# Optimization experiments

Measured on AMD Instinct MI355X. Metric: run time of the kernel, lower is better.

## Reference

```python
import jax, jax.numpy as jnp
import numpy as np

N = 50000
E = 800000
IN_F = 128
HID = 128
OUT_F = 64
MU = 2.0
EPS = 1e-12


def setup_inputs() -> dict:
    key = jax.random.key(0)
    ks = jax.random.split(key, 20)
    d = {}
    d["x"] = jax.random.normal(ks[0], (N, IN_F), dtype=jnp.float32)
    d["edge_src"] = jax.random.randint(ks[1], (E,), 0, N, dtype=jnp.int32)
    d["edge_dst"] = jax.random.randint(ks[2], (E,), 0, N, dtype=jnp.int32)
    d["edge_val"] = jax.random.uniform(ks[3], (E,), dtype=jnp.float32)
    # layer 0: in=128 -> pool=128 -> out=128 (activation=relu)
    s0 = 1.0 / np.sqrt(IN_F)
    d["pool_w0"] = jax.random.uniform(ks[4], (IN_F, IN_F), jnp.float32, -s0, s0)
    d["pool_b0"] = jax.random.uniform(ks[5], (IN_F,), jnp.float32, -s0, s0)
    d["fc1_w0"] = jax.random.uniform(ks[6], (HID, IN_F), jnp.float32, -s0, s0)
    d["fc1_b0"] = jax.random.uniform(ks[7], (HID,), jnp.float32, -s0, s0)
    d["fc2_w0"] = jax.random.uniform(ks[8], (HID, IN_F), jnp.float32, -s0, s0)
    d["fc2_b0"] = jax.random.uniform(ks[9], (HID,), jnp.float32, -s0, s0)
    # layer 1 (final): in=128 -> pool=128 -> out=64 (no activation)
    s1 = 1.0 / np.sqrt(HID)
    d["pool_w1"] = jax.random.uniform(ks[10], (HID, HID), jnp.float32, -s1, s1)
    d["pool_b1"] = jax.random.uniform(ks[11], (HID,), jnp.float32, -s1, s1)
    d["fc1_w1"] = jax.random.uniform(ks[12], (OUT_F, HID), jnp.float32, -s1, s1)
    d["fc1_b1"] = jax.random.uniform(ks[13], (OUT_F,), jnp.float32, -s1, s1)
    d["fc2_w1"] = jax.random.uniform(ks[14], (OUT_F, HID), jnp.float32, -s1, s1)
    d["fc2_b1"] = jax.random.uniform(ks[15], (OUT_F,), jnp.float32, -s1, s1)
    return d


def _sage_conv(x, src, dst, val, pw, pb, w1, b1, w2, b2, act):
    # L2-normalize rows (F.normalize(x, dim=1))
    xn = x / jnp.maximum(jnp.linalg.norm(x, axis=1, keepdims=True), EPS)
    h = jax.nn.relu(xn @ pw.T + pb)               # [N, pool]
    h_mu = h ** MU                                # elementwise pow
    # spmm(adj, h_mu): gather source rows, scale by edge weight, scatter-add to dst rows
    agg = jax.ops.segment_sum(h_mu[src] * val[:, None], dst, num_segments=N)
    agg = agg ** (1.0 / MU)                       # generalized-mean root
    out = (h @ w1.T + b1) + (agg @ w2.T + b2)
    return jax.nn.relu(out) if act else out


def reference(x, edge_src, edge_dst, edge_val,
              pool_w0, pool_b0, fc1_w0, fc1_b0, fc2_w0, fc2_b0,
              pool_w1, pool_b1, fc1_w1, fc1_b1, fc2_w1, fc2_b1):
    h = _sage_conv(x, edge_src, edge_dst, edge_val,
                   pool_w0, pool_b0, fc1_w0, fc1_b0, fc2_w0, fc2_b0, act=True)
    out = _sage_conv(h, edge_src, edge_dst, edge_val,
                     pool_w1, pool_b1, fc1_w1, fc1_b1, fc2_w1, fc2_b1, act=False)
    return out
```

## Files before the change

kernel.cpp:

```cpp
#include <hip/hip_runtime.h>

#define FF 128
#define BCAP 8192
#define CHUNK 4096

typedef __attribute__((ext_vector_type(8))) short short8;
typedef __attribute__((ext_vector_type(4))) float f32x4;

__device__ __forceinline__ unsigned short bf16_rne(float f) {
    unsigned u = __float_as_uint(f);
    u += 0x7fffu + ((u >> 16) & 1u);
    return (unsigned short)(u >> 16);
}
__device__ __forceinline__ float bf16_to_f32(unsigned short h) {
    return __uint_as_float(((unsigned)h) << 16);
}

template<int OUT, int PRE, int ADD, int RELU, int ABF16, int OUTBF16, int OUTSQ>
__global__ __launch_bounds__(256, 2)
void mm_mfma(const void* __restrict__ xin_,
             const unsigned short* __restrict__ Wh, const unsigned short* __restrict__ Wl,
             const float* __restrict__ bias, const float* __restrict__ addsrc,
             void* __restrict__ out_, unsigned short* __restrict__ hsq_out, int N)
{
    constexpr int PITCH = 136;
    __shared__ unsigned short sXh[64 * PITCH];
    __shared__ unsigned short sXl[ABF16 ? 1 : 64 * PITCH];

    const int tid  = threadIdx.x;
    const int tile = blockIdx.x;

    #pragma unroll
    for (int rg = 0; rg < 2; ++rg) {
        const int row = rg * 32 + (tid >> 3);
        const int c0  = (tid & 7) * 16;
        const int n   = tile * 64 + row;
        const int base = row * PITCH + c0;
        if constexpr (ABF16) {
            const unsigned short* xin = (const unsigned short*)xin_;
            short8 a = {0,0,0,0,0,0,0,0}, b = a;
            if (n < N) {
                const short8* p = (const short8*)(xin + (size_t)n * FF + c0);
                a = p[0]; b = p[1];
            }
            *(short8*)&sXh[base]     = a;
            *(short8*)&sXh[base + 8] = b;
        } else {
            const float* xin = (const float*)xin_;
            float v[16];
            if (n < N) {
                const float4* p = (const float4*)(xin + (size_t)n * FF + c0);
                #pragma unroll
                for (int i = 0; i < 4; ++i) {
                    float4 q = p[i];
                    v[4*i] = q.x; v[4*i+1] = q.y; v[4*i+2] = q.z; v[4*i+3] = q.w;
                }
            } else {
                #pragma unroll
                for (int i = 0; i < 16; ++i) v[i] = 0.f;
            }
            if constexpr (PRE == 1) {
                float ss = 0.f;
                #pragma unroll
                for (int i = 0; i < 16; ++i) ss = fmaf(v[i], v[i], ss);
                ss += __shfl_xor(ss, 1);
                ss += __shfl_xor(ss, 2);
                ss += __shfl_xor(ss, 4);
                float scl = 1.0f / fmaxf(sqrtf(ss), 1e-12f);
                #pragma unroll
                for (int i = 0; i < 16; ++i) v[i] *= scl;
            }
            union { unsigned short u[8]; short8 s; } h0, h1, l0, l1;
            #pragma unroll
            for (int i = 0; i < 8; ++i) {
                unsigned short ha = bf16_rne(v[i]);
                unsigned short hb = bf16_rne(v[8 + i]);
                h0.u[i] = ha; h1.u[i] = hb;
                l0.u[i] = bf16_rne(v[i]     - bf16_to_f32(ha));
                l1.u[i] = bf16_rne(v[8 + i] - bf16_to_f32(hb));
            }
            *(short8*)&sXh[base]     = h0.s;
            *(short8*)&sXh[base + 8] = h1.s;
            *(short8*)&sXl[base]     = l0.s;
            *(short8*)&sXl[base + 8] = l1.s;
        }
    }
    __syncthreads();

    const int lane = tid & 63, wave = tid >> 6;
    const int quad = lane >> 4, l16 = lane & 15;
    constexpr int CT = (OUT == 128) ? 2 : 1;

    short8 Bh[CT][4], Bl[CT][4];
    #pragma unroll
    for (int c = 0; c < CT; ++c) {
        const int jt = (OUT == 128) ? (2 * wave + c) : wave;
        #pragma unroll
        for (int t = 0; t < 4; ++t) {
            const size_t o = ((size_t)(jt * 4 + t) * 64 + lane) * 8;
            Bh[c][t] = *(const short8*)&Wh[o];
            Bl[c][t] = *(const short8*)&Wl[o];
        }
    }

    f32x4 acc[4][CT];
    #pragma unroll
    for (int r = 0; r < 4; ++r)
        #pragma unroll
        for (int c = 0; c < CT; ++c) {
            f32x4 z = {0.f, 0.f, 0.f, 0.f};
            acc[r][c] = z;
        }

    #pragma unroll
    for (int t = 0; t < 4; ++t) {
        short8 Ah[4], Al[4];
        #pragma unroll
        for (int r = 0; r < 4; ++r) {
            const int off = (r * 16 + l16) * PITCH + t * 32 + quad * 8;
            Ah[r] = *(const short8*)&sXh[off];
            if constexpr (!ABF16) Al[r] = *(const short8*)&sXl[off];
        }
        #pragma unroll
        for (int c = 0; c < CT; ++c)
            #pragma unroll
            for (int r = 0; r < 4; ++r) {
                acc[r][c] = __builtin_amdgcn_mfma_f32_16x16x32_bf16(Ah[r], Bh[c][t], acc[r][c], 0, 0, 0);
                if constexpr (!ABF16)
                    acc[r][c] = __builtin_amdgcn_mfma_f32_16x16x32_bf16(Al[r], Bh[c][t], acc[r][c], 0, 0, 0);
                acc[r][c] = __builtin_amdgcn_mfma_f32_16x16x32_bf16(Ah[r], Bl[c][t], acc[r][c], 0, 0, 0);
            }
    }

    #pragma unroll
    for (int c = 0; c < CT; ++c) {
        const int jt = (OUT == 128) ? (2 * wave + c) : wave;
        const int j = jt * 16 + l16;
        const float bj = bias[j];
        #pragma unroll
        for (int r = 0; r < 4; ++r) {
            #pragma unroll
            for (int g = 0; g < 4; ++g) {
                const int n = tile * 64 + r * 16 + quad * 4 + g;
                if (n < N) {
                    float val = acc[r][c][g] + bj;
                    if constexpr (ADD) val += addsrc[(size_t)n * OUT + j];
                    if constexpr (RELU) val = fmaxf(val, 0.f);
                    if constexpr (OUTBF16)
                        ((unsigned short*)out_)[(size_t)n * OUT + j] = bf16_rne(val);
                    else
                        ((float*)out_)[(size_t)n * OUT + j] = val;
                    if constexpr (OUTSQ)
                        hsq_out[(size_t)n * OUT + j] = bf16_rne(val * val);
                }
            }
        }
    }
}

template<int OUT, int RELU>
__global__ __launch_bounds__(256, 2)
void mm2_mfma(const unsigned short* __restrict__ hin,
              const unsigned short* __restrict__ aggh,
              const unsigned short* __restrict__ W1h, const unsigned short* __restrict__ W1l,
              const unsigned short* __restrict__ W2h, const unsigned short* __restrict__ W2l,
              const float* __restrict__ b1, const float* __restrict__ b2,
              float* __restrict__ out_, int N)
{
    constexpr int PITCH = 136;
    __shared__ unsigned short sH [64 * PITCH];
    __shared__ unsigned short sAh[64 * PITCH];

    const int tid  = threadIdx.x;
    const int tile = blockIdx.x;

    #pragma unroll
    for (int rg = 0; rg < 2; ++rg) {
        const int row = rg * 32 + (tid >> 3);
        const int c0  = (tid & 7) * 16;
        const int n   = tile * 64 + row;
        const int base = row * PITCH + c0;
        short8 z = {0,0,0,0,0,0,0,0};
        short8 a = z, b = z, c = z, d = z;
        if (n < N) {
            const short8* ph = (const short8*)(hin  + (size_t)n * FF + c0);
            const short8* pa = (const short8*)(aggh + (size_t)n * FF + c0);
            a = ph[0]; b = ph[1];
            c = pa[0]; d = pa[1];
        }
        *(short8*)&sH [base]     = a;
        *(short8*)&sH [base + 8] = b;
        *(short8*)&sAh[base]     = c;
        *(short8*)&sAh[base + 8] = d;
    }
    __syncthreads();

    const int lane = tid & 63, wave = tid >> 6;
    const int quad = lane >> 4, l16 = lane & 15;
    constexpr int CT = (OUT == 128) ? 2 : 1;

    short8 B1hf[CT][4], B1lf[CT][4], B2hf[CT][4], B2lf[CT][4];
    #pragma unroll
    for (int c = 0; c < CT; ++c) {
        const int jt = (OUT == 128) ? (2 * wave + c) : wave;
        #pragma unroll
        for (int t = 0; t < 4; ++t) {
            const size_t o = ((size_t)(jt * 4 + t) * 64 + lane) * 8;
            B1hf[c][t] = *(const short8*)&W1h[o];
            B1lf[c][t] = *(const short8*)&W1l[o];
            B2hf[c][t] = *(const short8*)&W2h[o];
            B2lf[c][t] = *(const short8*)&W2l[o];
        }
    }

    f32x4 acc[4][CT];
    #pragma unroll
    for (int r = 0; r < 4; ++r)
        #pragma unroll
        for (int c = 0; c < CT; ++c) {
            f32x4 z = {0.f, 0.f, 0.f, 0.f};
            acc[r][c] = z;
        }

    #pragma unroll
    for (int t = 0; t < 4; ++t) {
        short8 Hf[4], AH[4];
        #pragma unroll
        for (int r = 0; r < 4; ++r) {
            const int off = (r * 16 + l16) * PITCH + t * 32 + quad * 8;
            Hf[r] = *(const short8*)&sH[off];
            AH[r] = *(const short8*)&sAh[off];
        }
        #pragma unroll
        for (int c = 0; c < CT; ++c)
            #pragma unroll
            for (int r = 0; r < 4; ++r) {
                acc[r][c] = __builtin_amdgcn_mfma_f32_16x16x32_bf16(Hf[r], B1hf[c][t], acc[r][c], 0, 0, 0);
                acc[r][c] = __builtin_amdgcn_mfma_f32_16x16x32_bf16(Hf[r], B1lf[c][t], acc[r][c], 0, 0, 0);
                acc[r][c] = __builtin_amdgcn_mfma_f32_16x16x32_bf16(AH[r], B2hf[c][t], acc[r][c], 0, 0, 0);
                acc[r][c] = __builtin_amdgcn_mfma_f32_16x16x32_bf16(AH[r], B2lf[c][t], acc[r][c], 0, 0, 0);
            }
    }

    #pragma unroll
    for (int c = 0; c < CT; ++c) {
        const int jt = (OUT == 128) ? (2 * wave + c) : wave;
        const int j = jt * 16 + l16;
        const float bj = b1[j] + b2[j];
        #pragma unroll
        for (int r = 0; r < 4; ++r) {
            #pragma unroll
            for (int g = 0; g < 4; ++g) {
                const int n = tile * 64 + r * 16 + quad * 4 + g;
                if (n < N) {
                    float val = acc[r][c][g] + bj;
                    if constexpr (RELU) val = fmaxf(val, 0.f);
                    out_[(size_t)n * OUT + j] = val;
                }
            }
        }
    }
}

struct WPack {
    const float* src[6];
    unsigned short* hi[6];
    unsigned short* lo[6];
    int n[6];
};

__global__ __launch_bounds__(256)
void wprep_kernel(WPack p, int* __restrict__ bucket_cnt)
{
    if (blockIdx.x == 0) bucket_cnt[threadIdx.x] = 0;
    int id = blockIdx.x * 256 + threadIdx.x;
    #pragma unroll
    for (int i = 0; i < 6; ++i) {
        if (id < p.n[i]) {
            float f = p.src[i][id];
            unsigned short h = bf16_rne(f);
            const int j = id >> 7, k = id & 127;
            const int jt = j >> 4, l16 = j & 15;
            const int t = k >> 5, quad = (k >> 3) & 3, j8 = k & 7;
            const size_t o = ((size_t)((jt * 4 + t) * 4 + quad) * 16 + l16) * 8 + j8;
            p.hi[i][o] = h;
            p.lo[i][o] = bf16_rne(f - bf16_to_f32(h));
            return;
        }
        id -= p.n[i];
    }
}

__global__ __launch_bounds__(256)
void partA_kernel(const int* __restrict__ src, const int* __restrict__ dst,
                  const float* __restrict__ val, int* __restrict__ bucket_cnt,
                  int2* __restrict__ ebuf, int E)
{
    __shared__ int cnt[256], sc[256], excl[256], cur[256], gbase[256];
    __shared__ int2 staged[CHUNK];
    const int t = threadIdx.x;
    const int e0 = blockIdx.x * CHUNK;
    const int n  = min(CHUNK, E - e0);

    cnt[t] = 0;
    __syncthreads();
    for (int i = t; i < n; i += 256)
        atomicAdd(&cnt[((unsigned)dst[e0 + i]) >> 8], 1);
    __syncthreads();

    sc[t] = cnt[t];
    __syncthreads();
    #pragma unroll
    for (int off = 1; off < 256; off <<= 1) {
        int v = (t >= off) ? sc[t - off] : 0;
        __syncthreads();
        sc[t] += v;
        __syncthreads();
    }
    excl[t] = sc[t] - cnt[t];
    cur[t]  = excl[t];
    if (cnt[t] > 0) gbase[t] = atomicAdd(&bucket_cnt[t], cnt[t]);
    __syncthreads();

    for (int i = t; i < n; i += 256) {
        int d = dst[e0 + i];
        int s = src[e0 + i];
        float v = val[e0 + i];
        int b = ((unsigned)d) >> 8;
        int slot = atomicAdd(&cur[b], 1);
        staged[slot] = make_int2((s & 0xffff) | (d << 16), __float_as_int(v));
    }
    __syncthreads();

    for (int p = t; p < n; p += 256) {
        int2 ent = staged[p];
        int b = ((unsigned)ent.x) >> 24;
        int gpos = gbase[b] + (p - excl[b]);
        ebuf[(size_t)b * BCAP + gpos] = ent;
    }
}

__global__ __launch_bounds__(256)
void partB_kernel(const int* __restrict__ bucket_cnt, const int2* __restrict__ ebuf,
                  int* __restrict__ offsets, int2* __restrict__ edata,
                  int N, int E, int nbuck)
{
    __shared__ int pre[256], hist[256], sc[256], excl[256], cur[256];
    const int t = threadIdx.x;
    const int b = blockIdx.x;

    pre[t] = (t < nbuck) ? bucket_cnt[t] : 0;
    __syncthreads();
    #pragma unroll
    for (int off = 1; off < 256; off <<= 1) {
        int v = (t >= off) ? pre[t - off] : 0;
        __syncthreads();
        pre[t] += v;
        __syncthreads();
    }
    const int base = (b == 0) ? 0 : pre[b - 1];
    const int cnt  = pre[b] - base;

    hist[t] = 0;
    __syncthreads();
    const int2* ib = ebuf + (size_t)b * BCAP;
    for (int i = t; i < cnt; i += 256)
        atomicAdd(&hist[(((unsigned)ib[i].x) >> 16) & 255], 1);
    __syncthreads();

    sc[t] = hist[t];
    __syncthreads();
    #pragma unroll
    for (int off = 1; off < 256; off <<= 1) {
        int v = (t >= off) ? sc[t - off] : 0;
        __syncthreads();
        sc[t] += v;
        __syncthreads();
    }
    excl[t] = sc[t] - hist[t];
    cur[t]  = excl[t];

    const int node = b * 256 + t;
    if (node <= N) offsets[node] = base + excl[t];
    __syncthreads();

    for (int i = t; i < cnt; i += 256) {
        int2 ent = ib[i];
        int l = (((unsigned)ent.x) >> 16) & 255;
        int pos = base + atomicAdd(&cur[l], 1);
        edata[pos] = make_int2(ent.x & 0xffff, ent.y);
    }
}

__device__ __forceinline__ void fma4(float4& a, float v, uint2 u) {
    a.x = fmaf(v, __uint_as_float(u.x << 16), a.x);
    a.y = fmaf(v, __uint_as_float(u.x & 0xffff0000u), a.y);
    a.z = fmaf(v, __uint_as_float(u.y << 16), a.z);
    a.w = fmaf(v, __uint_as_float(u.y & 0xffff0000u), a.w);
}

__global__ __launch_bounds__(256)
void agg_kernel(const unsigned short* __restrict__ hsq, const int* __restrict__ offsets,
                const int2* __restrict__ edata,
                unsigned short* __restrict__ aggh, int N)
{
    const int w = blockIdx.x * 8 + (threadIdx.x >> 5);
    if (w >= N) return;
    const int l = threadIdx.x & 31;
    const size_t fo = (size_t)(l * 4);
    int e = offsets[w];
    const int end = offsets[w + 1];

    float4 a0 = {0,0,0,0}, a1 = {0,0,0,0}, a2 = {0,0,0,0}, a3 = {0,0,0,0};

    if ((e & 1) && e < end) {
        int2 ed = edata[e];
        uint2 u = *(const uint2*)&hsq[(size_t)ed.x * FF + fo];
        fma4(a0, __int_as_float(ed.y), u);
        ++e;
    }
    for (; e + 3 < end; e += 4) {
        int4 p0 = *(const int4*)&edata[e];
        int4 p1 = *(const int4*)&edata[e + 2];
        uint2 u0 = *(const uint2*)&hsq[(size_t)p0.x * FF + fo];
        uint2 u1 = *(const uint2*)&hsq[(size_t)p0.z * FF + fo];
        uint2 u2 = *(const uint2*)&hsq[(size_t)p1.x * FF + fo];
        uint2 u3 = *(const uint2*)&hsq[(size_t)p1.z * FF + fo];
        fma4(a0, __int_as_float(p0.y), u0);
        fma4(a1, __int_as_float(p0.w), u1);
        fma4(a2, __int_as_float(p1.y), u2);
        fma4(a3, __int_as_float(p1.w), u3);
    }
    if (e + 1 < end) {
        int4 p = *(const int4*)&edata[e];
        uint2 u0 = *(const uint2*)&hsq[(size_t)p.x * FF + fo];
        uint2 u1 = *(const uint2*)&hsq[(size_t)p.z * FF + fo];
        fma4(a0, __int_as_float(p.y), u0);
        fma4(a1, __int_as_float(p.w), u1);
        e += 2;
    }
    if (e < end) {
        int2 ed = edata[e];
        uint2 u = *(const uint2*)&hsq[(size_t)ed.x * FF + fo];
        fma4(a0, __int_as_float(ed.y), u);
    }

    float4 r;
    r.x = sqrtf(a0.x + a1.x + a2.x + a3.x);
    r.y = sqrtf(a0.y + a1.y + a2.y + a3.y);
    r.z = sqrtf(a0.z + a1.z + a2.z + a3.z);
    r.w = sqrtf(a0.w + a1.w + a2.w + a3.w);

    uint2 hv = { (unsigned)bf16_rne(r.x) | ((unsigned)bf16_rne(r.y) << 16),
                 (unsigned)bf16_rne(r.z) | ((unsigned)bf16_rne(r.w) << 16) };
    *(uint2*)&aggh[(size_t)w * FF + fo] = hv;
}

extern "C" void kernel_launch(void* const* d_in, const int* in_sizes, int n_in,
                              void* d_out, int out_size, void* d_ws, size_t ws_size,
                              hipStream_t stream) {
    const float* x    = (const float*)d_in[0];
    const int*   esrc = (const int*)d_in[1];
    const int*   edst = (const int*)d_in[2];
    const float* eval = (const float*)d_in[3];
    const float* pw0  = (const float*)d_in[4];
    const float* pb0  = (const float*)d_in[5];
    const float* f1w0 = (const float*)d_in[6];
    const float* f1b0 = (const float*)d_in[7];
    const float* f2w0 = (const float*)d_in[8];
    const float* f2b0 = (const float*)d_in[9];
    const float* pw1  = (const float*)d_in[10];
    const float* pb1  = (const float*)d_in[11];
    const float* f1w1 = (const float*)d_in[12];
    const float* f1b1 = (const float*)d_in[13];
    const float* f2w1 = (const float*)d_in[14];
    const float* f2b1 = (const float*)d_in[15];
    float* out = (float*)d_out;

    const int N = in_sizes[0] / FF;
    const int E = in_sizes[1];
    const int nbuck = (N + 255) / 256;

    char* ws = (char*)d_ws;
    const size_t rowsz = (size_t)N * FF * sizeof(float);
    const size_t A = 256;
    size_t off = 0;
    unsigned short* h    = (unsigned short*)(ws + off); off += (rowsz / 2 + A - 1) / A * A;
    unsigned short* hsq  = (unsigned short*)(ws + off); off += (rowsz / 2 + A - 1) / A * A;
    unsigned short* aggh = (unsigned short*)(ws + off); off += (rowsz / 2 + A - 1) / A * A;
    float* x1  = (float*)(ws + off); off += rowsz;
    int* offsets = (int*)(ws + off); off += ((size_t)(N + 1) * 4 + A - 1) / A * A;
    int* bucket_cnt = (int*)(ws + off); off += (size_t)256 * 4;
    int2* ebuf  = (int2*)(ws + off); off += (size_t)nbuck * BCAP * 8;
    int2* edata = (int2*)(ws + off); off += (size_t)E * 8;
    const int wsz[6] = {128 * FF, 128 * FF, 128 * FF, 128 * FF, 64 * FF, 64 * FF};
    unsigned short* whi[6];
    unsigned short* wlo[6];
    for (int i = 0; i < 6; ++i) {
        whi[i] = (unsigned short*)(ws + off); off += (size_t)wsz[i] * 2;
        wlo[i] = (unsigned short*)(ws + off); off += (size_t)wsz[i] * 2;
    }

    WPack pack;
    const float* wsrc[6] = {pw0, f1w0, f2w0, pw1, f1w1, f2w1};
    int wtotal = 0;
    for (int i = 0; i < 6; ++i) {
        pack.src[i] = wsrc[i]; pack.hi[i] = whi[i]; pack.lo[i] = wlo[i]; pack.n[i] = wsz[i];
        wtotal += wsz[i];
    }

    const int ntiles     = (N + 63) / 64;
    const int nodeblocks = (N + 7) / 8;
    dim3 B(256);

    wprep_kernel<<<(wtotal + 255) / 256, B, 0, stream>>>(pack, bucket_cnt);

    partA_kernel<<<(E + CHUNK - 1) / CHUNK, B, 0, stream>>>(esrc, edst, eval, bucket_cnt, ebuf, E);
    partB_kernel<<<nbuck, B, 0, stream>>>(bucket_cnt, ebuf, offsets, edata, N, E, nbuck);

    mm_mfma<128, 1, 0, 1, 0, 1, 1><<<ntiles, B, 0, stream>>>(x, whi[0], wlo[0], pb0, nullptr, h, hsq, N);
    agg_kernel<<<nodeblocks, B, 0, stream>>>(hsq, offsets, edata, aggh, N);
    mm2_mfma<128, 1><<<ntiles, B, 0, stream>>>(h, aggh, whi[1], wlo[1], whi[2], wlo[2], f1b0, f2b0, x1, N);

    mm_mfma<128, 1, 0, 1, 0, 1, 1><<<ntiles, B, 0, stream>>>(x1, whi[3], wlo[3], pb1, nullptr, h, hsq, N);
    agg_kernel<<<nodeblocks, B, 0, stream>>>(hsq, offsets, edata, aggh, N);
    mm2_mfma<64, 0><<<ntiles, B, 0, stream>>>(h, aggh, whi[4], wlo[4], whi[5], wlo[5], f1b1, f2b1, out, N);
}
```

Measured before the change: 257.2 us.

## Store layer-1 activations in bf16 and apply row normalization after the matmul

The intermediate layer-0 output x1 is now written as bf16 instead of fp32, halving its write and read traffic. The L2 row normalization moves to the epilogue: per-row inverse norms are kept in shared memory and applied as a scale on the accumulator, so the input is no longer split into hi/lo bf16 parts. This removes one of the three MFMAs per tile step and the low-part shared-memory plane. In exchange the activation input precision drops to single bf16, which adds rounding error.

```diff
diff --git a/kernel.cpp b/kernel.cpp
--- a/kernel.cpp
+++ b/kernel.cpp
@@ -16,16 +16,16 @@
     return __uint_as_float(((unsigned)h) << 16);
 }
 
-template<int OUT, int PRE, int ADD, int RELU, int ABF16, int OUTBF16, int OUTSQ>
+template<int ABF16>
 __global__ __launch_bounds__(256, 2)
-void mm_mfma(const void* __restrict__ xin_,
-             const unsigned short* __restrict__ Wh, const unsigned short* __restrict__ Wl,
-             const float* __restrict__ bias, const float* __restrict__ addsrc,
-             void* __restrict__ out_, unsigned short* __restrict__ hsq_out, int N)
+void pool_mfma(const void* __restrict__ xin_,
+               const unsigned short* __restrict__ Wh, const unsigned short* __restrict__ Wl,
+               const float* __restrict__ bias,
+               unsigned short* __restrict__ hout, unsigned short* __restrict__ hsqout, int N)
 {
     constexpr int PITCH = 136;
-    __shared__ unsigned short sXh[64 * PITCH];
-    __shared__ unsigned short sXl[ABF16 ? 1 : 64 * PITCH];
+    __shared__ unsigned short sX[64 * PITCH];
+    __shared__ float sNorm[64];
 
     const int tid  = threadIdx.x;
     const int tile = blockIdx.x;
@@ -36,15 +36,24 @@
         const int c0  = (tid & 7) * 16;
         const int n   = tile * 64 + row;
         const int base = row * PITCH + c0;
+        float ss = 0.f;
         if constexpr (ABF16) {
             const unsigned short* xin = (const unsigned short*)xin_;
-            short8 a = {0,0,0,0,0,0,0,0}, b = a;
+            union { short8 s; unsigned short u[8]; } a, b;
+            short8 z = {0,0,0,0,0,0,0,0};
+            a.s = z; b.s = z;
             if (n < N) {
                 const short8* p = (const short8*)(xin + (size_t)n * FF + c0);
-                a = p[0]; b = p[1];
-            }
-            *(short8*)&sXh[base]     = a;
-            *(short8*)&sXh[base + 8] = b;
+                a.s = p[0]; b.s = p[1];
+            }
+            #pragma unroll
+            for (int i = 0; i < 8; ++i) {
+                float fa = bf16_to_f32(a.u[i]);
+                float fb = bf16_to_f32(b.u[i]);
+                ss = fmaf(fa, fa, fmaf(fb, fb, ss));
+            }
+            *(short8*)&sX[base]     = a.s;
+            *(short8*)&sX[base + 8] = b.s;
         } else {
             const float* xin = (const float*)xin_;
             float v[16];
@@ -59,42 +68,31 @@
                 #pragma unroll
                 for (int i = 0; i < 16; ++i) v[i] = 0.f;
             }
-            if constexpr (PRE == 1) {
-                float ss = 0.f;
-                #pragma unroll
-                for (int i = 0; i < 16; ++i) ss = fmaf(v[i], v[i], ss);
-                ss += __shfl_xor(ss, 1);
-                ss += __shfl_xor(ss, 2);
-                ss += __shfl_xor(ss, 4);
-                float scl = 1.0f / fmaxf(sqrtf(ss), 1e-12f);
-                #pragma unroll
-                for (int i = 0; i < 16; ++i) v[i] *= scl;
-            }
-            union { unsigned short u[8]; short8 s; } h0, h1, l0, l1;
+            #pragma unroll
+            for (int i = 0; i < 16; ++i) ss = fmaf(v[i], v[i], ss);
+            union { unsigned short u[8]; short8 s; } h0, h1;
             #pragma unroll
             for (int i = 0; i < 8; ++i) {
-                unsigned short ha = bf16_rne(v[i]);
-                unsigned short hb = bf16_rne(v[8 + i]);
-                h0.u[i] = ha; h1.u[i] = hb;
-                l0.u[i] = bf16_rne(v[i]     - bf16_to_f32(ha));
-                l1.u[i] = bf16_rne(v[8 + i] - bf16_to_f32(hb));
-            }
-            *(short8*)&sXh[base]     = h0.s;
-            *(short8*)&sXh[base + 8] = h1.s;
-            *(short8*)&sXl[base]     = l0.s;
-            *(short8*)&sXl[base + 8] = l1.s;
-        }
+                h0.u[i] = bf16_rne(v[i]);
+                h1.u[i] = bf16_rne(v[8 + i]);
+            }
+            *(short8*)&sX[base]     = h0.s;
+            *(short8*)&sX[base + 8] = h1.s;
+        }
+        ss += __shfl_xor(ss, 1);
+        ss += __shfl_xor(ss, 2);
+        ss += __shfl_xor(ss, 4);
+        if ((tid & 7) == 0) sNorm[row] = 1.0f / fmaxf(sqrtf(ss), 1e-12f);
     }
     __syncthreads();
 
     const int lane = tid & 63, wave = tid >> 6;
     const int quad = lane >> 4, l16 = lane & 15;
-    constexpr int CT = (OUT == 128) ? 2 : 1;
-
-    short8 Bh[CT][4], Bl[CT][4];
-    #pragma unroll
-    for (int c = 0; c < CT; ++c) {
-        const int jt = (OUT == 128) ? (2 * wave + c) : wave;
+
+    short8 Bh[2][4], Bl[2][4];
+    #pragma unroll
+    for (int c = 0; c < 2; ++c) {
+        const int jt = 2 * wave + c;
         #pragma unroll
         for (int t = 0; t < 4; ++t) {
             const size_t o = ((size_t)(jt * 4 + t) * 64 + lane) * 8;
@@ -103,69 +101,60 @@
         }
     }
 
-    f32x4 acc[4][CT];
+    f32x4 acc[4][2];
     #pragma unroll
     for (int r = 0; r < 4; ++r)
         #pragma unroll
-        for (int c = 0; c < CT; ++c) {
+        for (int c = 0; c < 2; ++c) {
             f32x4 z = {0.f, 0.f, 0.f, 0.f};
             acc[r][c] = z;
         }
 
     #pragma unroll
     for (int t = 0; t < 4; ++t) {
-        short8 Ah[4], Al[4];
-        #pragma unroll
-        for (int r = 0; r < 4; ++r) {
-            const int off = (r * 16 + l16) * PITCH + t * 32 + quad * 8;
-            Ah[r] = *(const short8*)&sXh[off];
-            if constexpr (!ABF16) Al[r] = *(const short8*)&sXl[off];
-        }
-        #pragma unroll
-        for (int c = 0; c < CT; ++c)
+        short8 Ah[4];
+        #pragma unroll
+        for (int r = 0; r < 4; ++r)
+            Ah[r] = *(const short8*)&sX[(r * 16 + l16) * PITCH + t * 32 + quad * 8];
+        #pragma unroll
+        for (int c = 0; c < 2; ++c)
             #pragma unroll
             for (int r = 0; r < 4; ++r) {
                 acc[r][c] = __builtin_amdgcn_mfma_f32_16x16x32_bf16(Ah[r], Bh[c][t], acc[r][c], 0, 0, 0);
-                if constexpr (!ABF16)
-                    acc[r][c] = __builtin_amdgcn_mfma_f32_16x16x32_bf16(Al[r], Bh[c][t], acc[r][c], 0, 0, 0);
                 acc[r][c] = __builtin_amdgcn_mfma_f32_16x16x32_bf16(Ah[r], Bl[c][t], acc[r][c], 0, 0, 0);
             }
     }
 
     #pragma unroll
-    for (int c = 0; c < CT; ++c) {
-        const int jt = (OUT == 128) ? (2 * wave + c) : wave;
-        const int j = jt * 16 + l16;
+    for (int c = 0; c < 2; ++c) {
+        const int j = (2 * wave + c) * 16 + l16;
         const float bj = bias[j];
         #pragma unroll
         for (int r = 0; r < 4; ++r) {
             #pragma unroll
             for (int g = 0; g < 4; ++g) {
-                const int n = tile * 64 + r * 16 + quad * 4 + g;
+                const int nl = r * 16 + quad * 4 + g;
+                const int n = tile * 64 + nl;
                 if (n < N) {
-                    float val = acc[r][c][g] + bj;
-                    if constexpr (ADD) val += addsrc[(size_t)n * OUT + j];
-                    if constexpr (RELU) val = fmaxf(val, 0.f);
-                    if constexpr (OUTBF16)
-                        ((unsigned short*)out_)[(size_t)n * OUT + j] = bf16_rne(val);
-                    else
-                        ((float*)out_)[(size_t)n * OUT + j] = val;
-                    if constexpr (OUTSQ)
-                        hsq_out[(size_t)n * OUT + j] = bf16_rne(val * val);
+                    float s = sNorm[nl];
+                    float val = fmaf(acc[r][c][g], s, bj);
+                    val = fmaxf(val, 0.f);
+                    hout  [(size_t)n * FF + j] = bf16_rne(val);
+                    hsqout[(size_t)n * FF + j] = bf16_rne(val * val);
                 }
             }
         }
     }
 }
 
-template<int OUT, int RELU>
+template<int OUT, int RELU, int OUTBF16>
 __global__ __launch_bounds__(256, 2)
 void mm2_mfma(const unsigned short* __restrict__ hin,
               const unsigned short* __restrict__ aggh,
               const unsigned short* __restrict__ W1h, const unsigned short* __restrict__ W1l,
               const unsigned short* __restrict__ W2h, const unsigned short* __restrict__ W2l,
               const float* __restrict__ b1, const float* __restrict__ b2,
-              float* __restrict__ out_, int N)
+              void* __restrict__ out_, int N)
 {
     constexpr int PITCH = 136;
     __shared__ unsigned short sH [64 * PITCH];
@@ -255,7 +244,10 @@
                 if (n < N) {
                     float val = acc[r][c][g] + bj;
                     if constexpr (RELU) val = fmaxf(val, 0.f);
-                    out_[(size_t)n * OUT + j] = val;
+                    if constexpr (OUTBF16)
+                        ((unsigned short*)out_)[(size_t)n * OUT + j] = bf16_rne(val);
+                    else
+                        ((float*)out_)[(size_t)n * OUT + j] = val;
                 }
             }
         }
@@ -482,13 +474,13 @@
     const int nbuck = (N + 255) / 256;
 
     char* ws = (char*)d_ws;
-    const size_t rowsz = (size_t)N * FF * sizeof(float);
+    const size_t planesz = (size_t)N * FF * 2;
     const size_t A = 256;
     size_t off = 0;
-    unsigned short* h    = (unsigned short*)(ws + off); off += (rowsz / 2 + A - 1) / A * A;
-    unsigned short* hsq  = (unsigned short*)(ws + off); off += (rowsz / 2 + A - 1) / A * A;
-    unsigned short* aggh = (unsigned short*)(ws + off); off += (rowsz / 2 + A - 1) / A * A;
-    float* x1  = (float*)(ws + off); off += rowsz;
+    unsigned short* h    = (unsigned short*)(ws + off); off += (planesz + A - 1) / A * A;
+    unsigned short* hsq  = (unsigned short*)(ws + off); off += (planesz + A - 1) / A * A;
+    unsigned short* aggh = (unsigned short*)(ws + off); off += (planesz + A - 1) / A * A;
+    unsigned short* x1   = (unsigned short*)(ws + off); off += (planesz + A - 1) / A * A;
     int* offsets = (int*)(ws + off); off += ((size_t)(N + 1) * 4 + A - 1) / A * A;
     int* bucket_cnt = (int*)(ws + off); off += (size_t)256 * 4;
     int2* ebuf  = (int2*)(ws + off); off += (size_t)nbuck * BCAP * 8;
@@ -518,11 +510,11 @@
     partA_kernel<<<(E + CHUNK - 1) / CHUNK, B, 0, stream>>>(esrc, edst, eval, bucket_cnt, ebuf, E);
     partB_kernel<<<nbuck, B, 0, stream>>>(bucket_cnt, ebuf, offsets, edata, N, E, nbuck);
 
-    mm_mfma<128, 1, 0, 1, 0, 1, 1><<<ntiles, B, 0, stream>>>(x, whi[0], wlo[0], pb0, nullptr, h, hsq, N);
+    pool_mfma<0><<<ntiles, B, 0, stream>>>(x, whi[0], wlo[0], pb0, h, hsq, N);
     agg_kernel<<<nodeblocks, B, 0, stream>>>(hsq, offsets, edata, aggh, N);
-    mm2_mfma<128, 1><<<ntiles, B, 0, stream>>>(h, aggh, whi[1], wlo[1], whi[2], wlo[2], f1b0, f2b0, x1, N);
-
-    mm_mfma<128, 1, 0, 1, 0, 1, 1><<<ntiles, B, 0, stream>>>(x1, whi[3], wlo[3], pb1, nullptr, h, hsq, N);
+    mm2_mfma<128, 1, 1><<<ntiles, B, 0, stream>>>(h, aggh, whi[1], wlo[1], whi[2], wlo[2], f1b0, f2b0, x1, N);
+
+    pool_mfma<1><<<ntiles, B, 0, stream>>>(x1, whi[3], wlo[3], pb1, h, hsq, N);
     agg_kernel<<<nodeblocks, B, 0, stream>>>(hsq, offsets, edata, aggh, N);
-    mm2_mfma<64, 0><<<ntiles, B, 0, stream>>>(h, aggh, whi[4], wlo[4], whi[5], wlo[5], f1b1, f2b1, out, N);
-}
+    mm2_mfma<64, 0, 0><<<ntiles, B, 0, stream>>>(h, aggh, whi[4], wlo[4], whi[5], wlo[5], f1b1, f2b1, out, N);
+}
```

New measurement: 248.6 us. -3.4%, faster.
